# Kernel optimization log

Hardware: AMD Instinct MI355X
Metric: run time of the kernel (lower is better)

Reference implementation:

```python
import jax, jax.numpy as jnp
import numpy as np

B, N, D, H = 4, 1024, 1024, 8
HD = D // H  # head dim = 128


def _layernorm(x, g, b, eps=1e-5):
    mu = jnp.mean(x, axis=-1, keepdims=True)
    var = jnp.mean(jnp.square(x - mu), axis=-1, keepdims=True)
    return (x - mu) * jax.lax.rsqrt(var + eps) * g + b


def setup_inputs() -> dict:
    key = jax.random.key(0)
    ks = jax.random.split(key, 8)
    x = jax.random.normal(ks[0], (B, N, D), dtype=jnp.float32)
    adj = (jax.random.uniform(ks[1], (B, N, N)) < 0.02).astype(jnp.int32)
    adj = jnp.maximum(adj, jnp.eye(N, dtype=jnp.int32)[None])  # self-loops: no empty softmax rows
    stoich = jax.random.normal(ks[2], (B, N), dtype=jnp.float32)
    s = 0.02
    W1 = jax.random.normal(ks[3], (D, 4 * D), dtype=jnp.float32) * s
    W2 = jax.random.normal(ks[4], (4 * D, D), dtype=jnp.float32) * s
    gW = jax.random.normal(ks[5], (D,), dtype=jnp.float32) * s  # Linear(1, D) weight
    return {
        "x": x, "adj_matrix": adj, "stoichiometry": stoich,
        "ln1_g": jnp.ones((D,), jnp.float32), "ln1_b": jnp.zeros((D,), jnp.float32),
        "ln2_g": jnp.ones((D,), jnp.float32), "ln2_b": jnp.zeros((D,), jnp.float32),
        "W1": W1, "b1": jnp.zeros((4 * D,), jnp.float32),
        "W2": W2, "b2": jnp.zeros((D,), jnp.float32),
        "gW": gW, "gb": jnp.zeros((D,), jnp.float32),
    }


def reference(x, adj_matrix, stoichiometry, ln1_g, ln1_b, ln2_g, ln2_b, W1, b1, W2, b2, gW, gb):
    normed = _layernorm(x, ln1_g, ln1_b)
    # q = k = v = normed, split into heads: [B, H, N, HD]
    qkv = normed.reshape(B, N, H, HD).transpose(0, 2, 1, 3)
    scores = jnp.einsum("bhqd,bhkd->bhqk", qkv, qkv) / jnp.sqrt(jnp.float32(HD))
    # stoichiometry gate: Linear(1, D) + sigmoid -> [B, N, D]; broadcast as [B, 1, N, D] (D == N)
    gates = jax.nn.sigmoid(stoichiometry[:, :, None] * gW + gb)[:, None]  # [B,1,N,N]
    mask = adj_matrix[:, None] > 0  # [B,1,N,N]
    # gate only valid entries (equivalent to (-inf)*gate since gate>0), then mask
    masked = jnp.where(mask, scores * gates, -jnp.inf)
    attn = jax.nn.softmax(masked, axis=-1)
    out = jnp.einsum("bhqk,bhkd->bhqd", attn, qkv)
    out = out.transpose(0, 2, 1, 3).reshape(B, N, D)
    x = x + out
    normed2 = _layernorm(x, ln2_g, ln2_b)
    mlp = jax.nn.gelu(normed2 @ W1 + b1, approximate=False) @ W2 + b2
    return x + mlp
```

## Files before the change

kernel.cpp:

```cpp
#include <hip/hip_runtime.h>
#include <math.h>

#define NTOK 1024
#define DMODEL 1024
#define BATCH 4

typedef __bf16 bf16x8 __attribute__((ext_vector_type(8)));
typedef float  f32x4  __attribute__((ext_vector_type(4)));
typedef unsigned short ushort_t;
typedef unsigned short us8 __attribute__((ext_vector_type(8)));

static __device__ __forceinline__ ushort_t f2bf(float f) {
  unsigned u = __float_as_uint(f);
  u += 0x7fffu + ((u >> 16) & 1u);
  return (ushort_t)(u >> 16);
}
static __device__ __forceinline__ float bf2f(ushort_t v) {
  return __uint_as_float(((unsigned)v) << 16);
}

static __device__ __forceinline__ float fast_gelu(float v) {
  const float u = 1.5957691216057308f * (v + 0.044715f * v * v * v);
  return v / (1.f + __expf(-u));
}

static __device__ __forceinline__ void gld16(void* lds, const void* g) {
  __builtin_amdgcn_global_load_lds(
      (const __attribute__((address_space(1))) void*)g,
      (__attribute__((address_space(3))) void*)lds, 16, 0, 0);
}

__global__ __launch_bounds__(256) void prep_kernel(
    const float* __restrict__ x, const float* __restrict__ g,
    const float* __restrict__ b, ushort_t* __restrict__ out,
    const float* __restrict__ W1, ushort_t* __restrict__ W1t,
    const float* __restrict__ W2, ushort_t* __restrict__ W2t)
{
  if (blockIdx.x < 4096) {
    const int row = blockIdx.x;
    const int tid = threadIdx.x;
    const float* xr = x + (size_t)row * DMODEL;
    float4 v = *(const float4*)(xr + 4 * tid);
    float s1 = v.x + v.y + v.z + v.w;
    float s2 = v.x * v.x + v.y * v.y + v.z * v.z + v.w * v.w;
#pragma unroll
    for (int d = 1; d < 64; d <<= 1) { s1 += __shfl_xor(s1, d); s2 += __shfl_xor(s2, d); }
    __shared__ float red[10];
    const int wid = tid >> 6;
    if ((tid & 63) == 0) { red[wid] = s1; red[4 + wid] = s2; }
    __syncthreads();
    if (tid == 0) {
      float a = red[0] + red[1] + red[2] + red[3];
      float c = red[4] + red[5] + red[6] + red[7];
      float mu = a / (float)DMODEL;
      float var = c / (float)DMODEL - mu * mu;
      red[8] = mu; red[9] = rsqrtf(var + 1e-5f);
    }
    __syncthreads();
    const float mu = red[8], inv = red[9];
    float4 gg = *(const float4*)(g + 4 * tid);
    float4 bb = *(const float4*)(b + 4 * tid);
    ushort4 o;
    o.x = f2bf((v.x - mu) * inv * gg.x + bb.x);
    o.y = f2bf((v.y - mu) * inv * gg.y + bb.y);
    o.z = f2bf((v.z - mu) * inv * gg.z + bb.z);
    o.w = f2bf((v.w - mu) * inv * gg.w + bb.w);
    *(ushort4*)(out + (size_t)row * DMODEL + 4 * tid) = o;
  } else {
    __shared__ float t[32][33];
    int id = blockIdx.x - 4096;
    const float* W; ushort_t* Wt; int K, N, bx, by;
    if (id < 4096) { W = W1; Wt = W1t; K = 1024; N = 4096; bx = id & 127; by = id >> 7; }
    else { id -= 4096; W = W2; Wt = W2t; K = 4096; N = 1024; bx = id & 31; by = id >> 5; }
    const int kb = by * 32, nb = bx * 32;
    const int c = threadIdx.x & 31, r0 = threadIdx.x >> 5;
#pragma unroll
    for (int r = r0; r < 32; r += 8)
      t[r][c] = W[(size_t)(kb + r) * N + nb + c];
    __syncthreads();
#pragma unroll
    for (int r = r0; r < 32; r += 8)
      Wt[(size_t)(nb + r) * K + kb + c] = f2bf(t[c][r]);
  }
}

__global__ __launch_bounds__(256) void attn_kernel(
    const float* __restrict__ x, const ushort_t* __restrict__ normedB,
    const int* __restrict__ adj, const float* __restrict__ stoich,
    const float* __restrict__ gW, const float* __restrict__ gb,
    const float* __restrict__ ln2g, const float* __restrict__ ln2b,
    const float* __restrict__ b2,
    float* __restrict__ outbase, ushort_t* __restrict__ normed2)
{
  __shared__ int   neigh[2][NTOK];
  __shared__ float gateS[2][NTOK];
  __shared__ int   cntS[2];
  __shared__ float red[2][6];

  const int tid = threadIdx.x;
  const int sub = tid >> 7;
  const int t   = tid & 127;
  const int row = blockIdx.x * 2 + sub;
  const int b   = row >> 10;

  if (tid < 2) cntS[tid] = 0;
  __syncthreads();
  const int* arow = adj + (size_t)row * NTOK;
  {
    int4 a4 = ((const int4*)arow)[t];
    int k0 = 4 * t;
    if (a4.x > 0) { int p = atomicAdd(&cntS[sub], 1); neigh[sub][p] = k0; }
    if (a4.y > 0) { int p = atomicAdd(&cntS[sub], 1); neigh[sub][p] = k0 + 1; }
    if (a4.z > 0) { int p = atomicAdd(&cntS[sub], 1); neigh[sub][p] = k0 + 2; }
    if (a4.w > 0) { int p = atomicAdd(&cntS[sub], 1); neigh[sub][p] = k0 + 3; }
    a4 = ((const int4*)arow)[t + 128];
    k0 = 4 * (t + 128);
    if (a4.x > 0) { int p = atomicAdd(&cntS[sub], 1); neigh[sub][p] = k0; }
    if (a4.y > 0) { int p = atomicAdd(&cntS[sub], 1); neigh[sub][p] = k0 + 1; }
    if (a4.z > 0) { int p = atomicAdd(&cntS[sub], 1); neigh[sub][p] = k0 + 2; }
    if (a4.w > 0) { int p = atomicAdd(&cntS[sub], 1); neigh[sub][p] = k0 + 3; }
  }
  __syncthreads();
  const int cnt = cntS[sub];

  const float st = stoich[row];
  for (int i = t; i < cnt; i += 128) {
    int k = neigh[sub][i];
    gateS[sub][i] = 1.f / (1.f + __expf(-fmaf(st, gW[k], gb[k])));
  }
  __syncthreads();

  const ushort_t* nbB = normedB + (size_t)b * NTOK * DMODEL;
  const int d0 = 8 * t;
  us8 qu = *(const us8*)(nbB + (size_t)(row & 1023) * DMODEL + d0);
  float qv[8];
#pragma unroll
  for (int j = 0; j < 8; ++j) qv[j] = bf2f(qu[j]);
  const float scale = 0.08838834764831845f;

  float lsum = 0.f;
  float o[8] = {0.f, 0.f, 0.f, 0.f, 0.f, 0.f, 0.f, 0.f};

  for (int i0 = 0; i0 < cnt; i0 += 8) {
    us8 ku[8]; float w8[8];
#pragma unroll
    for (int u = 0; u < 8; ++u) {
      const int i = i0 + u;
      const int ii = (i < cnt) ? i : 0;
      ku[u] = *(const us8*)(nbB + (size_t)neigh[sub][ii] * DMODEL + d0);
      w8[u] = gateS[sub][ii];
    }
#pragma unroll
    for (int u = 0; u < 8; ++u) {
      float p = 0.f;
#pragma unroll
      for (int j = 0; j < 8; ++j) p = fmaf(bf2f(ku[u][j]), qv[j], p);
      p += __shfl_xor(p, 1); p += __shfl_xor(p, 2);
      p += __shfl_xor(p, 4); p += __shfl_xor(p, 8);
      w8[u] *= p * scale;
    }
#pragma unroll
    for (int u = 0; u < 8; ++u)
      w8[u] = (i0 + u < cnt) ? __expf(w8[u]) : 0.f;
#pragma unroll
    for (int u = 0; u < 8; ++u) {
      lsum += w8[u];
#pragma unroll
      for (int j = 0; j < 8; ++j) o[j] = fmaf(w8[u], bf2f(ku[u][j]), o[j]);
    }
  }
  const float pinv = 1.f / lsum;

  const float* xr = x + (size_t)row * DMODEL + d0;
  const float4 xa = *(const float4*)(xr);
  const float4 xb = *(const float4*)(xr + 4);
  float r[8];
  r[0] = xa.x + o[0] * pinv; r[1] = xa.y + o[1] * pinv;
  r[2] = xa.z + o[2] * pinv; r[3] = xa.w + o[3] * pinv;
  r[4] = xb.x + o[4] * pinv; r[5] = xb.y + o[5] * pinv;
  r[6] = xb.z + o[6] * pinv; r[7] = xb.w + o[7] * pinv;

  const float4 ba = *(const float4*)(b2 + d0);
  const float4 bbv = *(const float4*)(b2 + d0 + 4);
  float4 oa, ob;
  oa.x = r[0] + ba.x;  oa.y = r[1] + ba.y;  oa.z = r[2] + ba.z;  oa.w = r[3] + ba.w;
  ob.x = r[4] + bbv.x; ob.y = r[5] + bbv.y; ob.z = r[6] + bbv.z; ob.w = r[7] + bbv.w;
  float* obp = outbase + (size_t)row * DMODEL + d0;
  *(float4*)(obp) = oa;
  *(float4*)(obp + 4) = ob;

  float s1 = 0.f, s2 = 0.f;
#pragma unroll
  for (int j = 0; j < 8; ++j) { s1 += r[j]; s2 += r[j] * r[j]; }
#pragma unroll
  for (int d = 1; d < 64; d <<= 1) { s1 += __shfl_xor(s1, d); s2 += __shfl_xor(s2, d); }
  const int wsub = (tid >> 6) & 1;
  if ((tid & 63) == 0) { red[sub][wsub] = s1; red[sub][2 + wsub] = s2; }
  __syncthreads();
  if ((tid & 127) == 0) {
    float a = red[sub][0] + red[sub][1];
    float c = red[sub][2] + red[sub][3];
    float mu = a / (float)DMODEL;
    float var = c / (float)DMODEL - mu * mu;
    red[sub][4] = mu; red[sub][5] = rsqrtf(var + 1e-5f);
  }
  __syncthreads();
  const float mu = red[sub][4], inv = red[sub][5];
  const float4 ga = *(const float4*)(ln2g + d0);
  const float4 gbv = *(const float4*)(ln2g + d0 + 4);
  const float4 la = *(const float4*)(ln2b + d0);
  const float4 lb = *(const float4*)(ln2b + d0 + 4);
  const float gg[8] = {ga.x, ga.y, ga.z, ga.w, gbv.x, gbv.y, gbv.z, gbv.w};
  const float ll[8] = {la.x, la.y, la.z, la.w, lb.x, lb.y, lb.z, lb.w};
  us8 pk;
#pragma unroll
  for (int j = 0; j < 8; ++j) pk[j] = f2bf((r[j] - mu) * inv * gg[j] + ll[j]);
  *(us8*)(normed2 + (size_t)row * DMODEL + d0) = pk;
}

__global__ __launch_bounds__(512, 2) void gemm1_pipe(
    const ushort_t* __restrict__ A, const ushort_t* __restrict__ Bt,
    const float* __restrict__ bias, ushort_t* __restrict__ Cout,
    int M, int N, int K)
{
  __shared__ __align__(16) ushort_t As[2][256 * 64];
  __shared__ __align__(16) ushort_t Bs[2][256 * 64];

  const int id = blockIdx.x;
  const int xcd = id & 7, slot = id >> 3;
  const int bm = (xcd * 2 + (slot >> 4)) * 256;
  const int bn = (slot & 15) * 256;

  const int tid = threadIdx.x;
  const int l = tid & 63;
  const int wid = tid >> 6;
  const int wrow = (wid >> 2) * 128;
  const int wcol = (wid & 3) * 64;

  const int sr = tid >> 3;
  const int sg = tid & 7;
  const int gsrc = ((sg ^ (sr & 7)) << 3);
  const ushort_t* Ag = A  + (size_t)(bm + sr) * K + gsrc;
  const ushort_t* Bg = Bt + (size_t)(bn + sr) * K + gsrc;
  const int dst = tid * 8;

  const int quad = l >> 4, lrow = l & 15;
  const int swz = lrow & 7;
  const int gx0 = ((quad ^ swz) << 3);
  const int gx1 = (((quad + 4) ^ swz) << 3);

  f32x4 acc[8][4] = {};
  bf16x8 bfr[4];

#define STAGE8(buf, kb)                                                        \
  gld16(&As[buf][0 * 4096 + dst], Ag + (size_t)0 * 64 * K + (kb));             \
  gld16(&As[buf][1 * 4096 + dst], Ag + (size_t)1 * 64 * K + (kb));             \
  gld16(&As[buf][2 * 4096 + dst], Ag + (size_t)2 * 64 * K + (kb));             \
  gld16(&As[buf][3 * 4096 + dst], Ag + (size_t)3 * 64 * K + (kb));             \
  gld16(&Bs[buf][0 * 4096 + dst], Bg + (size_t)0 * 64 * K + (kb));             \
  gld16(&Bs[buf][1 * 4096 + dst], Bg + (size_t)1 * 64 * K + (kb));             \
  gld16(&Bs[buf][2 * 4096 + dst], Bg + (size_t)2 * 64 * K + (kb));             \
  gld16(&Bs[buf][3 * 4096 + dst], Bg + (size_t)3 * 64 * K + (kb));

#define QUARTER(buf, GX, IH, LB)                                               \
  {                                                                            \
    if (LB) {                                                                  \
      _Pragma("unroll")                                                        \
      for (int j = 0; j < 4; ++j) {                                            \
        const int rb = wcol + j * 16 + lrow;                                   \
        bfr[j] = *(const bf16x8*)(&Bs[buf][rb * 64 + (GX)]);                   \
      }                                                                        \
    }                                                                          \
    bf16x8 af[4];                                                              \
    _Pragma("unroll")                                                          \
    for (int ii = 0; ii < 4; ++ii) {                                           \
      const int ra = wrow + (IH) * 64 + ii * 16 + lrow;                        \
      af[ii] = *(const bf16x8*)(&As[buf][ra * 64 + (GX)]);                     \
    }                                                                          \
    __builtin_amdgcn_s_setprio(1);                                             \
    _Pragma("unroll")                                                          \
    for (int ii = 0; ii < 4; ++ii)                                             \
      _Pragma("unroll")                                                        \
      for (int j = 0; j < 4; ++j)                                              \
        acc[(IH) * 4 + ii][j] = __builtin_amdgcn_mfma_f32_16x16x32_bf16(       \
            af[ii], bfr[j], acc[(IH) * 4 + ii][j], 0, 0, 0);                   \
    __builtin_amdgcn_s_setprio(0);                                             \
  }

  STAGE8(0, 0);

  const int NTK = K >> 6;
#pragma unroll 1
  for (int t = 0; t < NTK - 1; ++t) {
    const int cb = t & 1, nb = cb ^ 1;
    STAGE8(nb, (t + 1) << 6);
    asm volatile("s_waitcnt vmcnt(8)" ::: "memory");
    __builtin_amdgcn_s_barrier();
    __builtin_amdgcn_sched_barrier(0);
    QUARTER(cb, gx0, 0, 1);
    QUARTER(cb, gx0, 1, 0);
    QUARTER(cb, gx1, 0, 1);
    QUARTER(cb, gx1, 1, 0);
    __builtin_amdgcn_s_barrier();
  }
  {
    const int cb = (NTK - 1) & 1;
    asm volatile("s_waitcnt vmcnt(0)" ::: "memory");
    __builtin_amdgcn_s_barrier();
    __builtin_amdgcn_sched_barrier(0);
    QUARTER(cb, gx0, 0, 1);
    QUARTER(cb, gx0, 1, 0);
    QUARTER(cb, gx1, 0, 1);
    QUARTER(cb, gx1, 1, 0);
  }
#undef STAGE8
#undef QUARTER

#pragma unroll
  for (int i = 0; i < 8; ++i) {
    const int row0 = bm + wrow + 16 * i + quad * 4;
#pragma unroll
    for (int j = 0; j < 4; ++j) {
      const int col = bn + wcol + 16 * j + lrow;
      const float bi = bias[col];
#pragma unroll
      for (int r = 0; r < 4; ++r)
        Cout[(size_t)(row0 + r) * N + col] = f2bf(fast_gelu(acc[i][j][r] + bi));
    }
  }
}

__global__ __launch_bounds__(256, 2) void gemm2_pipe(
    const ushort_t* __restrict__ A, const ushort_t* __restrict__ Bt,
    float* __restrict__ Cout, int M, int N, int K, int kchunk)
{
  __shared__ __align__(16) ushort_t As[2][128 * 64];
  __shared__ __align__(16) ushort_t Bs[2][128 * 64];

  const int id = blockIdx.x;
  const int xcd = id & 7, slot = id >> 3;
  const int bm = (xcd * 4 + (slot & 3)) * 128;
  const int bn = ((slot >> 2) & 7) * 128;
  const int koff = (slot >> 5) * kchunk;

  const int tid = threadIdx.x;
  const int l = tid & 63;
  const int wid = tid >> 6;
  const int wm = (wid >> 1) * 64, wn = (wid & 1) * 64;

  const int sr = tid >> 3;
  const int sg = tid & 7;
  const int gsrc = ((sg ^ (sr & 7)) << 3);
  const ushort_t* Ag = A  + (size_t)(bm + sr) * K + koff + gsrc;
  const ushort_t* Bg = Bt + (size_t)(bn + sr) * K + koff + gsrc;
  const int dst = tid * 8;

  const int quad = l >> 4, lrow = l & 15;
  const int swz = lrow & 7;
  const int gx0 = ((quad ^ swz) << 3);
  const int gx1 = (((quad + 4) ^ swz) << 3);

  f32x4 acc[4][4] = {};

#define STAGE8K(buf, kb)                                                       \
  gld16(&As[buf][0 * 2048 + dst], Ag + (size_t)0 * 32 * K + (kb));             \
  gld16(&As[buf][1 * 2048 + dst], Ag + (size_t)1 * 32 * K + (kb));             \
  gld16(&As[buf][2 * 2048 + dst], Ag + (size_t)2 * 32 * K + (kb));             \
  gld16(&As[buf][3 * 2048 + dst], Ag + (size_t)3 * 32 * K + (kb));             \
  gld16(&Bs[buf][0 * 2048 + dst], Bg + (size_t)0 * 32 * K + (kb));             \
  gld16(&Bs[buf][1 * 2048 + dst], Bg + (size_t)1 * 32 * K + (kb));             \
  gld16(&Bs[buf][2 * 2048 + dst], Bg + (size_t)2 * 32 * K + (kb));             \
  gld16(&Bs[buf][3 * 2048 + dst], Bg + (size_t)3 * 32 * K + (kb));

#define HALF(buf, GX)                                                          \
  {                                                                            \
    bf16x8 af[4], bfv[4];                                                      \
    _Pragma("unroll")                                                          \
    for (int i = 0; i < 4; ++i)                                                \
      af[i] = *(const bf16x8*)(&As[buf][(wm + i * 16 + lrow) * 64 + (GX)]);    \
    _Pragma("unroll")                                                          \
    for (int j = 0; j < 4; ++j)                                                \
      bfv[j] = *(const bf16x8*)(&Bs[buf][(wn + j * 16 + lrow) * 64 + (GX)]);   \
    __builtin_amdgcn_s_setprio(1);                                             \
    _Pragma("unroll")                                                          \
    for (int i = 0; i < 4; ++i)                                                \
      _Pragma("unroll")                                                        \
      for (int j = 0; j < 4; ++j)                                              \
        acc[i][j] = __builtin_amdgcn_mfma_f32_16x16x32_bf16(                   \
            af[i], bfv[j], acc[i][j], 0, 0, 0);                                \
    __builtin_amdgcn_s_setprio(0);                                             \
  }

  STAGE8K(0, 0);

  const int NTK = kchunk >> 6;
#pragma unroll 1
  for (int t = 0; t < NTK - 1; ++t) {
    const int cb = t & 1, nb = cb ^ 1;
    STAGE8K(nb, (t + 1) << 6);
    asm volatile("s_waitcnt vmcnt(8)" ::: "memory");
    __builtin_amdgcn_s_barrier();
    __builtin_amdgcn_sched_barrier(0);
    HALF(cb, gx0);
    HALF(cb, gx1);
    __builtin_amdgcn_s_barrier();
  }
  {
    const int cb = (NTK - 1) & 1;
    asm volatile("s_waitcnt vmcnt(0)" ::: "memory");
    __builtin_amdgcn_s_barrier();
    __builtin_amdgcn_sched_barrier(0);
    HALF(cb, gx0);
    HALF(cb, gx1);
  }
#undef STAGE8K
#undef HALF

#pragma unroll
  for (int i = 0; i < 4; ++i) {
    const int row0 = bm + wm + 16 * i + quad * 4;
#pragma unroll
    for (int j = 0; j < 4; ++j) {
      const int col = bn + wn + 16 * j + lrow;
#pragma unroll
      for (int r = 0; r < 4; ++r)
        atomicAdd(&Cout[(size_t)(row0 + r) * N + col], acc[i][j][r]);
    }
  }
}

extern "C" void kernel_launch(void* const* d_in, const int* in_sizes, int n_in,
                              void* d_out, int out_size, void* d_ws, size_t ws_size,
                              hipStream_t stream) {
  const float* x      = (const float*)d_in[0];
  const int*   adj    = (const int*)d_in[1];
  const float* stoich = (const float*)d_in[2];
  const float* ln1g   = (const float*)d_in[3];
  const float* ln1b   = (const float*)d_in[4];
  const float* ln2g   = (const float*)d_in[5];
  const float* ln2b   = (const float*)d_in[6];
  const float* W1     = (const float*)d_in[7];
  const float* b1     = (const float*)d_in[8];
  const float* W2     = (const float*)d_in[9];
  const float* b2     = (const float*)d_in[10];
  const float* gW     = (const float*)d_in[11];
  const float* gb     = (const float*)d_in[12];
  float* out = (float*)d_out;
  char* ws = (char*)d_ws;

  ushort_t* normedB = (ushort_t*)(ws);
  ushort_t* normed2 = (ushort_t*)(ws + (16u << 20));
  ushort_t* hidden  = (ushort_t*)(ws + (24u << 20));
  ushort_t* W1t     = (ushort_t*)(ws + (56u << 20));
  ushort_t* W2t     = (ushort_t*)(ws + (64u << 20));

  const int ROWS = BATCH * NTOK;

  prep_kernel<<<12288, 256, 0, stream>>>(x, ln1g, ln1b, normedB,
                                         W1, W1t, W2, W2t);
  attn_kernel<<<ROWS / 2, 256, 0, stream>>>(x, normedB, adj, stoich, gW, gb,
                                            ln2g, ln2b, b2, out, normed2);
  gemm1_pipe<<<256, 512, 0, stream>>>(normed2, W1t, b1, hidden,
                                      ROWS, 4096, 1024);
  gemm2_pipe<<<512, 256, 0, stream>>>(hidden, W2t, out,
                                      ROWS, 1024, 4096, 2048);
}
```

Before: 259.3 us.

## Drop split-K in second MLP GEMM, use 512-thread blocks with plain accumulate

The second MLP GEMM no longer splits K across two blocks. Each of 256 blocks of 512 threads now covers the full K=4096 for one 128x128 tile, with eight waves each computing a 64x32 subtile. Because only one block writes each output element, the float atomicAdd epilogue becomes a plain read-add-write onto the residual already in out. The cost is half as many blocks and twice as many serial K iterations per block, which may lower parallelism and latency hiding on the GPU.

```diff
diff --git a/kernel.cpp b/kernel.cpp
--- a/kernel.cpp
+++ b/kernel.cpp
@@ -330,9 +330,9 @@
   }
 }
 
-__global__ __launch_bounds__(256, 2) void gemm2_pipe(
+__global__ __launch_bounds__(512, 2) void gemm2_pipe(
     const ushort_t* __restrict__ A, const ushort_t* __restrict__ Bt,
-    float* __restrict__ Cout, int M, int N, int K, int kchunk)
+    float* __restrict__ Cout, int M, int N, int K)
 {
   __shared__ __align__(16) ushort_t As[2][128 * 64];
   __shared__ __align__(16) ushort_t Bs[2][128 * 64];
@@ -340,19 +340,19 @@
   const int id = blockIdx.x;
   const int xcd = id & 7, slot = id >> 3;
   const int bm = (xcd * 4 + (slot & 3)) * 128;
-  const int bn = ((slot >> 2) & 7) * 128;
-  const int koff = (slot >> 5) * kchunk;
+  const int bn = (slot >> 2) * 128;
 
   const int tid = threadIdx.x;
   const int l = tid & 63;
   const int wid = tid >> 6;
-  const int wm = (wid >> 1) * 64, wn = (wid & 1) * 64;
+  const int wrow = (wid >> 2) * 64;
+  const int wcol = (wid & 3) * 32;
 
   const int sr = tid >> 3;
   const int sg = tid & 7;
   const int gsrc = ((sg ^ (sr & 7)) << 3);
-  const ushort_t* Ag = A  + (size_t)(bm + sr) * K + koff + gsrc;
-  const ushort_t* Bg = Bt + (size_t)(bn + sr) * K + koff + gsrc;
+  const ushort_t* Ag = A  + (size_t)(bm + sr) * K + gsrc;
+  const ushort_t* Bg = Bt + (size_t)(bn + sr) * K + gsrc;
   const int dst = tid * 8;
 
   const int quad = l >> 4, lrow = l & 15;
@@ -360,49 +360,45 @@
   const int gx0 = ((quad ^ swz) << 3);
   const int gx1 = (((quad + 4) ^ swz) << 3);
 
-  f32x4 acc[4][4] = {};
-
-#define STAGE8K(buf, kb)                                                       \
-  gld16(&As[buf][0 * 2048 + dst], Ag + (size_t)0 * 32 * K + (kb));             \
-  gld16(&As[buf][1 * 2048 + dst], Ag + (size_t)1 * 32 * K + (kb));             \
-  gld16(&As[buf][2 * 2048 + dst], Ag + (size_t)2 * 32 * K + (kb));             \
-  gld16(&As[buf][3 * 2048 + dst], Ag + (size_t)3 * 32 * K + (kb));             \
-  gld16(&Bs[buf][0 * 2048 + dst], Bg + (size_t)0 * 32 * K + (kb));             \
-  gld16(&Bs[buf][1 * 2048 + dst], Bg + (size_t)1 * 32 * K + (kb));             \
-  gld16(&Bs[buf][2 * 2048 + dst], Bg + (size_t)2 * 32 * K + (kb));             \
-  gld16(&Bs[buf][3 * 2048 + dst], Bg + (size_t)3 * 32 * K + (kb));
-
-#define HALF(buf, GX)                                                          \
+  f32x4 acc[4][2] = {};
+
+#define STAGE4(buf, kb)                                                        \
+  gld16(&As[buf][dst],        Ag + (kb));                                      \
+  gld16(&As[buf][4096 + dst], Ag + (size_t)64 * K + (kb));                     \
+  gld16(&Bs[buf][dst],        Bg + (kb));                                      \
+  gld16(&Bs[buf][4096 + dst], Bg + (size_t)64 * K + (kb));
+
+#define HALFK(buf, GX)                                                         \
   {                                                                            \
-    bf16x8 af[4], bfv[4];                                                      \
+    bf16x8 af[4], bfv[2];                                                      \
     _Pragma("unroll")                                                          \
     for (int i = 0; i < 4; ++i)                                                \
-      af[i] = *(const bf16x8*)(&As[buf][(wm + i * 16 + lrow) * 64 + (GX)]);    \
+      af[i] = *(const bf16x8*)(&As[buf][(wrow + i * 16 + lrow) * 64 + (GX)]);  \
     _Pragma("unroll")                                                          \
-    for (int j = 0; j < 4; ++j)                                                \
-      bfv[j] = *(const bf16x8*)(&Bs[buf][(wn + j * 16 + lrow) * 64 + (GX)]);   \
+    for (int j = 0; j < 2; ++j)                                                \
+      bfv[j] = *(const bf16x8*)(&Bs[buf][(wcol + j * 16 + lrow) * 64 + (GX)]); \
     __builtin_amdgcn_s_setprio(1);                                             \
     _Pragma("unroll")                                                          \
     for (int i = 0; i < 4; ++i)                                                \
       _Pragma("unroll")                                                        \
-      for (int j = 0; j < 4; ++j)                                              \
+      for (int j = 0; j < 2; ++j)                                              \
         acc[i][j] = __builtin_amdgcn_mfma_f32_16x16x32_bf16(                   \
             af[i], bfv[j], acc[i][j], 0, 0, 0);                                \
     __builtin_amdgcn_s_setprio(0);                                             \
   }
 
-  STAGE8K(0, 0);
-
-  const int NTK = kchunk >> 6;
+  STAGE4(0, 0);
+
+  const int NTK = K >> 6;
 #pragma unroll 1
   for (int t = 0; t < NTK - 1; ++t) {
     const int cb = t & 1, nb = cb ^ 1;
-    STAGE8K(nb, (t + 1) << 6);
-    asm volatile("s_waitcnt vmcnt(8)" ::: "memory");
+    STAGE4(nb, (t + 1) << 6);
+    asm volatile("s_waitcnt vmcnt(4)" ::: "memory");
     __builtin_amdgcn_s_barrier();
     __builtin_amdgcn_sched_barrier(0);
-    HALF(cb, gx0);
-    HALF(cb, gx1);
+    HALFK(cb, gx0);
+    HALFK(cb, gx1);
     __builtin_amdgcn_s_barrier();
   }
   {
@@ -410,21 +406,23 @@
     asm volatile("s_waitcnt vmcnt(0)" ::: "memory");
     __builtin_amdgcn_s_barrier();
     __builtin_amdgcn_sched_barrier(0);
-    HALF(cb, gx0);
-    HALF(cb, gx1);
-  }
-#undef STAGE8K
-#undef HALF
+    HALFK(cb, gx0);
+    HALFK(cb, gx1);
+  }
+#undef STAGE4
+#undef HALFK
 
 #pragma unroll
   for (int i = 0; i < 4; ++i) {
-    const int row0 = bm + wm + 16 * i + quad * 4;
-#pragma unroll
-    for (int j = 0; j < 4; ++j) {
-      const int col = bn + wn + 16 * j + lrow;
-#pragma unroll
-      for (int r = 0; r < 4; ++r)
-        atomicAdd(&Cout[(size_t)(row0 + r) * N + col], acc[i][j][r]);
+    const int row0 = bm + wrow + 16 * i + quad * 4;
+#pragma unroll
+    for (int j = 0; j < 2; ++j) {
+      const int col = bn + wcol + 16 * j + lrow;
+#pragma unroll
+      for (int r = 0; r < 4; ++r) {
+        float* p = &Cout[(size_t)(row0 + r) * N + col];
+        *p = *p + acc[i][j][r];
+      }
     }
   }
 }
@@ -462,6 +460,6 @@
                                             ln2g, ln2b, b2, out, normed2);
   gemm1_pipe<<<256, 512, 0, stream>>>(normed2, W1t, b1, hidden,
                                       ROWS, 4096, 1024);
-  gemm2_pipe<<<512, 256, 0, stream>>>(hidden, W2t, out,
-                                      ROWS, 1024, 4096, 2048);
-}
+  gemm2_pipe<<<256, 512, 0, stream>>>(hidden, W2t, out,
+                                      ROWS, 1024, 4096);
+}
```

Result: slower. 264.8 us (+2.1%).
